# Performance work log

Hardware: AMD Instinct MI355X
Metric: run time of the kernel (lower is better)

Reference implementation:

```python
import jax, jax.numpy as jnp
import numpy as np

H1, C1 = 16, 8   # layer1 heads, per-head channels
H2, C2 = 16, 8   # layer2 heads, per-head channels
NEG_SLOPE = 0.2


def _gatv2_layer(x, src, dst, Wl, Wr, att, bias, n_nodes, H, C):
    # x: [N, F]; Wl/Wr: [F, H*C]; att: [H, C]; bias: [H*C]
    xl = (x @ Wl).reshape(n_nodes, H, C)  # source transform
    xr = (x @ Wr).reshape(n_nodes, H, C)  # target transform
    e = jax.nn.leaky_relu(xl[src] + xr[dst], NEG_SLOPE)   # [E, H, C]
    logit = jnp.einsum('ehc,hc->eh', e, att)              # [E, H]
    # segment softmax over incoming edges of each target node
    m = jax.ops.segment_max(logit, dst, num_segments=n_nodes)  # [N, H]
    ex = jnp.exp(logit - m[dst])
    denom = jax.ops.segment_sum(ex, dst, num_segments=n_nodes)  # [N, H]
    alpha = ex / (denom[dst] + 1e-16)                     # [E, H]
    msg = xl[src] * alpha[..., None]                      # [E, H, C]
    out = jax.ops.segment_sum(msg, dst, num_segments=n_nodes)  # [N, H, C]
    return out.reshape(n_nodes, H * C) + bias


def setup_inputs() -> dict:
    key = jax.random.key(0)
    ks = jax.random.split(key, 10)
    N, E, F_IN = 50000, 800000, 128
    x = jax.random.normal(ks[0], (N, F_IN), dtype=jnp.float32)
    edge_index = jax.random.randint(ks[1], (2, E), 0, N, dtype=jnp.int32)
    s = 0.1
    return {
        'x': x,
        'edge_index': edge_index,
        'Wl1': jax.random.normal(ks[2], (F_IN, H1 * C1), dtype=jnp.float32) * s,
        'Wr1': jax.random.normal(ks[3], (F_IN, H1 * C1), dtype=jnp.float32) * s,
        'att1': jax.random.normal(ks[4], (H1, C1), dtype=jnp.float32) * s,
        'b1': jax.random.normal(ks[5], (H1 * C1,), dtype=jnp.float32) * s,
        'Wl2': jax.random.normal(ks[6], (H1 * C1, H2 * C2), dtype=jnp.float32) * s,
        'Wr2': jax.random.normal(ks[7], (H1 * C1, H2 * C2), dtype=jnp.float32) * s,
        'att2': jax.random.normal(ks[8], (H2, C2), dtype=jnp.float32) * s,
        'b2': jax.random.normal(ks[9], (H2 * C2,), dtype=jnp.float32) * s,
    }


def reference(x, edge_index, Wl1, Wr1, att1, b1, Wl2, Wr2, att2, b2):
    N = x.shape[0]
    # PyG GATv2Conv adds self-loops by default
    loops = jnp.arange(N, dtype=edge_index.dtype)
    src = jnp.concatenate([edge_index[0], loops])
    dst = jnp.concatenate([edge_index[1], loops])
    # eval mode: F.dropout(training=False) is identity
    h = _gatv2_layer(x, src, dst, Wl1, Wr1, att1, b1, N, H1, C1)
    h = jax.nn.elu(h)
    h = _gatv2_layer(h, src, dst, Wl2, Wr2, att2, b2, N, H2, C2)
    return jax.nn.log_softmax(h, axis=1)
```

## Files before the change

### kernel.cpp

```cpp
#include <hip/hip_runtime.h>

#define NEG_SLOPE 0.2f
#define BSHIFT 9
#define BNODES 512
#define EPB 2048
#define SCAP 10240
#define LOG2E 1.44269504088896340736f

typedef __attribute__((ext_vector_type(8))) short short8;
typedef __attribute__((ext_vector_type(4))) float f32x4;

__device__ inline ushort f2bf(float f) {
  uint u = __builtin_bit_cast(uint, f);
  uint r = (u + 0x7FFFu + ((u >> 16) & 1u)) >> 16;
  return (ushort)r;
}
__device__ inline float bclo(uint u) { return __builtin_bit_cast(float, u << 16); }
__device__ inline float bchi(uint u) { return __builtin_bit_cast(float, u & 0xFFFF0000u); }

__device__ inline float fast_exp2(float x) {
  float r;
  asm("v_exp_f32 %0, %1" : "=v"(r) : "v"(x));
  return r;
}

__global__ __launch_bounds__(256) void k_prep_pc(
    const float* __restrict__ Wl1, const float* __restrict__ Wr1,
    const float* __restrict__ Wl2, const float* __restrict__ Wr2,
    ushort* __restrict__ WT1, ushort* __restrict__ WT2,
    const int* __restrict__ edst, int E, int* __restrict__ gcount) {
  int bid = blockIdx.x;
  int t = threadIdx.x;
  if (bid < 256) {
    const float* Wa = (bid < 128) ? Wl1 : Wl2;
    const float* Wb = (bid < 128) ? Wr1 : Wr2;
    ushort* WT = (bid < 128) ? WT1 : WT2;
    int i = (bid & 127) * 256 + t;
    int n = i >> 7, k = i & 127;
    float v = (n < 128) ? Wa[k * 128 + n] : Wb[k * 128 + (n - 128)];
    WT[i] = f2bf(v);
  } else {
    __shared__ int hist[128];
    if (t < 128) hist[t] = 0;
    __syncthreads();
    int e0 = (bid - 256) * EPB;
#pragma unroll
    for (int k = 0; k < EPB / 256; ++k) {
      int e = e0 + k * 256 + t;
      if (e < E) atomicAdd(&hist[edst[e] >> BSHIFT], 1);
    }
    __syncthreads();
    if (t < 128 && hist[t] > 0) atomicAdd(&gcount[t], hist[t]);
  }
}

__global__ __launch_bounds__(256) void k_pscan(const int* __restrict__ gcount,
                                               int* __restrict__ bbase,
                                               int* __restrict__ gcursor, int nb) {
  __shared__ int tsum[256];
  int t = threadIdx.x;
  int v = (t < nb) ? gcount[t] : 0;
  tsum[t] = v;
  __syncthreads();
  for (int d = 1; d < 256; d <<= 1) {
    int x = (t >= d) ? tsum[t - d] : 0;
    __syncthreads();
    tsum[t] += x;
    __syncthreads();
  }
  int excl = tsum[t] - v;
  if (t < nb) { bbase[t] = excl; gcursor[t] = excl; }
  if (t == nb - 1) bbase[nb] = excl + v;
}

__global__ __launch_bounds__(256) void k_pscatter(const int* __restrict__ esrc,
                                                  const int* __restrict__ edst, int E,
                                                  int* __restrict__ gcursor,
                                                  uint* __restrict__ pairs) {
  __shared__ int hist[128], lbase[128], gbase[128];
  __shared__ int tsum[256];
  __shared__ uint stag[EPB];
  int t = threadIdx.x;
  if (t < 128) hist[t] = 0;
  __syncthreads();
  int e0 = blockIdx.x * EPB;
  int b[8], r[8];
  uint pp[8];
#pragma unroll
  for (int k = 0; k < 8; ++k) {
    int e = e0 + k * 256 + t;
    if (e < E) {
      int d = edst[e], s = esrc[e];
      pp[k] = ((uint)d << 16) | (uint)s;
      b[k] = d >> BSHIFT;
      r[k] = atomicAdd(&hist[b[k]], 1);
    } else b[k] = -1;
  }
  __syncthreads();
  int hv = (t < 128) ? hist[t] : 0;
  tsum[t] = hv;
  __syncthreads();
  for (int dd = 1; dd < 256; dd <<= 1) {
    int x = (t >= dd) ? tsum[t - dd] : 0;
    __syncthreads();
    tsum[t] += x;
    __syncthreads();
  }
  if (t < 128) lbase[t] = tsum[t] - hv;
  __syncthreads();
  int tot = tsum[255];
#pragma unroll
  for (int k = 0; k < 8; ++k)
    if (b[k] >= 0) stag[lbase[b[k]] + r[k]] = pp[k];
  if (t < 128 && hv > 0) gbase[t] = atomicAdd(&gcursor[t], hv);
  __syncthreads();
  for (int i = t; i < tot; i += 256) {
    uint p = stag[i];
    int bb = (int)(p >> (16 + BSHIFT));
    pairs[gbase[bb] + (i - lbase[bb])] = p;
  }
}

__global__ __launch_bounds__(256) void k_bsort(const uint* __restrict__ pairs,
                                               const int* __restrict__ bbase,
                                               int* __restrict__ csr, int* __restrict__ offs,
                                               int N, int nb) {
  __shared__ int hist[BNODES], cur[BNODES], tsum[256];
  __shared__ int sorted[SCAP];
  int t = threadIdx.x;
  int first = blockIdx.x << BSHIFT;
  int nn = min(BNODES, N - first);
  int base = bbase[blockIdx.x];
  int cnt = bbase[blockIdx.x + 1] - base;
  int cbase = blockIdx.x * SCAP;
  hist[t] = 0; hist[t + 256] = 0;
  __syncthreads();
  for (int i = t; i < cnt; i += 256)
    atomicAdd(&hist[(int)(pairs[base + i] >> 16) - first], 1);
  __syncthreads();
  int a0 = hist[2 * t], a1 = hist[2 * t + 1];
  int a0p = (a0 + 3) & ~3, a1p = (a1 + 3) & ~3;
  tsum[t] = a0p + a1p;
  __syncthreads();
  for (int dd = 1; dd < 256; dd <<= 1) {
    int x = (t >= dd) ? tsum[t - dd] : 0;
    __syncthreads();
    tsum[t] += x;
    __syncthreads();
  }
  int ex = tsum[t] - (a0p + a1p);
  cur[2 * t] = ex; cur[2 * t + 1] = ex + a0p;
  if (2 * t < nn)     offs[first + 2 * t]     = ((cbase + ex) << 8) | a0;
  if (2 * t + 1 < nn) offs[first + 2 * t + 1] = ((cbase + ex + a0p) << 8) | a1;
  __syncthreads();
  for (int i = t; i < cnt; i += 256) {
    uint p = pairs[base + i];
    int pos = atomicAdd(&cur[(int)(p >> 16) - first], 1);
    sorted[pos] = (int)(p & 0xFFFFu);
  }
  __syncthreads();
  int tot = tsum[255];
  for (int i = t; i < tot; i += 256) csr[cbase + i] = sorted[i];
}

template <bool F32IN>
__global__ __launch_bounds__(256) void k_gemm_mfma(
    const void* __restrict__ Xin, const ushort* __restrict__ WT,
    ushort* __restrict__ XLB, ushort* __restrict__ XRB, int N) {
  __shared__ ushort As[64 * 128];
  int tid = threadIdx.x;
  int lane = tid & 63;
  int w = tid >> 6;
  int n0 = blockIdx.x * 64;
  int wcol = w * 64;

  short8 bfrag[4][4];
#pragma unroll
  for (int nt = 0; nt < 4; ++nt)
#pragma unroll
    for (int ks = 0; ks < 4; ++ks)
      bfrag[nt][ks] = *reinterpret_cast<const short8*>(
          WT + (size_t)(wcol + nt * 16 + (lane & 15)) * 128 + ks * 32 + (lane >> 4) * 8);

#pragma unroll
  for (int it = 0; it < 4; ++it) {
    int flat = it * 256 + tid;
    int r = flat >> 4;
    int cb = (flat & 15) << 4;
    short8 v = {0, 0, 0, 0, 0, 0, 0, 0};
    int row = n0 + r;
    if (row < N) {
      if constexpr (F32IN) {
        const float* Xf = (const float*)Xin + (size_t)row * 128 + (cb >> 1);
        float4 f0 = *reinterpret_cast<const float4*>(Xf);
        float4 f1 = *reinterpret_cast<const float4*>(Xf + 4);
        v[0] = (short)f2bf(f0.x); v[1] = (short)f2bf(f0.y);
        v[2] = (short)f2bf(f0.z); v[3] = (short)f2bf(f0.w);
        v[4] = (short)f2bf(f1.x); v[5] = (short)f2bf(f1.y);
        v[6] = (short)f2bf(f1.z); v[7] = (short)f2bf(f1.w);
      } else {
        v = *reinterpret_cast<const short8*>((const ushort*)Xin +
                                             (size_t)row * 128 + (cb >> 1));
      }
    }
    *reinterpret_cast<short8*>(reinterpret_cast<char*>(As) + r * 256 +
                               (cb ^ ((r & 7) << 4))) = v;
  }
  __syncthreads();

  f32x4 acc[4][4];
#pragma unroll
  for (int mt = 0; mt < 4; ++mt)
#pragma unroll
    for (int nt = 0; nt < 4; ++nt) acc[mt][nt] = f32x4{0.f, 0.f, 0.f, 0.f};

#pragma unroll
  for (int ks = 0; ks < 4; ++ks) {
    short8 af[4];
#pragma unroll
    for (int mt = 0; mt < 4; ++mt) {
      int row = mt * 16 + (lane & 15);
      int cb = ks * 64 + (lane >> 4) * 16;
      af[mt] = *reinterpret_cast<const short8*>(
          reinterpret_cast<char*>(As) + row * 256 + (cb ^ ((row & 7) << 4)));
    }
#pragma unroll
    for (int mt = 0; mt < 4; ++mt)
#pragma unroll
      for (int nt = 0; nt < 4; ++nt)
        acc[mt][nt] = __builtin_amdgcn_mfma_f32_16x16x32_bf16(
            af[mt], bfrag[nt][ks], acc[mt][nt], 0, 0, 0);
  }

  ushort* dstp = (w < 2) ? XLB : XRB;
#pragma unroll
  for (int mt = 0; mt < 4; ++mt) {
    int rbase = n0 + mt * 16 + (lane >> 4) * 4;
#pragma unroll
    for (int nt = 0; nt < 4; ++nt) {
      int c = (wcol + nt * 16 + (lane & 15)) & 127;
#pragma unroll
      for (int r = 0; r < 4; ++r) {
        float v = acc[mt][nt][r];
        ushort mb = f2bf(v);
        uint ob = (uint)__shfl_xor((int)(uint)mb, 1);
        int row = rbase + r;
        if ((lane & 1) == 0 && row < N) {
          ushort2 st; st.x = mb; st.y = (ushort)ob;
          *reinterpret_cast<ushort2*>(dstp + (size_t)row * 128 + c) = st;
        }
      }
    }
  }
}

template <int MODE>
__global__ __launch_bounds__(256, 4) void k_aggregate(
    const ushort* __restrict__ XLB, const ushort* __restrict__ XRB,
    const int* __restrict__ offs, const int* __restrict__ csr,
    const float* __restrict__ att, const float* __restrict__ bias,
    void* __restrict__ OUTV, int N) {
  int tid = threadIdx.x;
  int lane = tid & 63;
  int grp = lane >> 4, li = lane & 15;
  int wid = (blockIdx.x * 256 + tid) >> 6;
  int node = (wid << 2) + grp;
  bool valid = node < N;
  int cnode = valid ? node : (N - 1);
  int ch = li << 3;

  float4 alo = *reinterpret_cast<const float4*>(att + ch);
  float4 ahi = *reinterpret_cast<const float4*>(att + ch + 4);
  const float C6 = 0.6f * LOG2E;
  float a60 = alo.x * C6, a61 = alo.y * C6, a62 = alo.z * C6, a63 = alo.w * C6;
  float a64 = ahi.x * C6, a65 = ahi.y * C6, a66 = ahi.z * C6, a67 = ahi.w * C6;
  const float TT = 0.66666667f;

  uint4 xru = *reinterpret_cast<const uint4*>(XRB + ((size_t)cnode << 7) + ch);
  float xr0 = bclo(xru.x), xr1 = bchi(xru.x), xr2 = bclo(xru.y), xr3 = bchi(xru.y);
  float xr4 = bclo(xru.z), xr5 = bchi(xru.z), xr6 = bclo(xru.w), xr7 = bchi(xru.w);

  float acc0 = 0.f, acc1 = 0.f, acc2 = 0.f, acc3 = 0.f;
  float acc4 = 0.f, acc5 = 0.f, acc6 = 0.f, acc7 = 0.f, den = 0.f;

  uint sd = (uint)offs[cnode];
  int e0 = (int)(sd >> 8);
  int deg = valid ? (int)(sd & 255u) : 0;
  int wmax = deg;
  wmax = max(wmax, __shfl_xor(wmax, 16));
  wmax = max(wmax, __shfl_xor(wmax, 32));
  int ITER = (wmax + 3) >> 2;

  const int4* csr4 = reinterpret_cast<const int4*>(csr + e0);

#define PROC(U4, ACT)                                                        \
  {                                                                          \
    float x0 = bclo((U4).x), x1 = bchi((U4).x);                              \
    float x2 = bclo((U4).y), x3 = bchi((U4).y);                              \
    float x4 = bclo((U4).z), x5 = bchi((U4).z);                              \
    float x6 = bclo((U4).w), x7 = bchi((U4).w);                              \
    float t0 = x0 + xr0, t1 = x1 + xr1, t2 = x2 + xr2, t3 = x3 + xr3;        \
    float t4 = x4 + xr4, t5 = x5 + xr5, t6 = x6 + xr6, t7 = x7 + xr7;        \
    float u0 = fmaf(fabsf(t0), TT, t0), u1 = fmaf(fabsf(t1), TT, t1);        \
    float u2 = fmaf(fabsf(t2), TT, t2), u3 = fmaf(fabsf(t3), TT, t3);        \
    float u4 = fmaf(fabsf(t4), TT, t4), u5 = fmaf(fabsf(t5), TT, t5);        \
    float u6 = fmaf(fabsf(t6), TT, t6), u7 = fmaf(fabsf(t7), TT, t7);        \
    float q = u0 * a60;                                                      \
    q = fmaf(u1, a61, q); q = fmaf(u2, a62, q); q = fmaf(u3, a63, q);        \
    q = fmaf(u4, a64, q); q = fmaf(u5, a65, q); q = fmaf(u6, a66, q);        \
    q = fmaf(u7, a67, q);                                                    \
    q = (ACT) ? q : -200.f;                                                  \
    float exv = fast_exp2(q);                                                \
    acc0 = fmaf(exv, x0, acc0); acc1 = fmaf(exv, x1, acc1);                  \
    acc2 = fmaf(exv, x2, acc2); acc3 = fmaf(exv, x3, acc3);                  \
    acc4 = fmaf(exv, x4, acc4); acc5 = fmaf(exv, x5, acc5);                  \
    acc6 = fmaf(exv, x6, acc6); acc7 = fmaf(exv, x7, acc7);                  \
    den += exv;                                                              \
  }

#define GATHER(B0, B1, B2, B3, IDX, I0)                                      \
  {                                                                          \
    int s0_ = ((I0) < deg) ? (IDX).x : cnode;                                \
    int s1_ = ((I0) + 1 < deg) ? (IDX).y : cnode;                            \
    int s2_ = ((I0) + 2 < deg) ? (IDX).z : cnode;                            \
    int s3_ = ((I0) + 3 < deg) ? (IDX).w : cnode;                            \
    B0 = *reinterpret_cast<const uint4*>(XLB + (((size_t)(uint)s0_) << 7) + ch); \
    B1 = *reinterpret_cast<const uint4*>(XLB + (((size_t)(uint)s1_) << 7) + ch); \
    B2 = *reinterpret_cast<const uint4*>(XLB + (((size_t)(uint)s2_) << 7) + ch); \
    B3 = *reinterpret_cast<const uint4*>(XLB + (((size_t)(uint)s3_) << 7) + ch); \
  }

#define PROC4(B0, B1, B2, B3, I0)                                            \
  {                                                                          \
    PROC(B0, (I0) < deg); PROC(B1, (I0) + 1 < deg);                          \
    PROC(B2, (I0) + 2 < deg); PROC(B3, (I0) + 3 < deg);                      \
  }

  {
    uint4 us = *reinterpret_cast<const uint4*>(XLB + ((size_t)cnode << 7) + ch);
    PROC(us, valid);
  }

  uint4 A0, A1, A2, A3, B0, B1, B2, B3;
  int4 ia, ib;
  if (ITER > 0) {
    ia = csr4[0];
    GATHER(A0, A1, A2, A3, ia, 0);
    ib = (ITER > 1) ? csr4[1] : ia;
    int b = 1;
    for (; b + 1 < ITER; b += 2) {
      GATHER(B0, B1, B2, B3, ib, 4 * b);
      ia = csr4[b + 1];
      PROC4(A0, A1, A2, A3, 4 * (b - 1));
      GATHER(A0, A1, A2, A3, ia, 4 * (b + 1));
      ib = csr4[b + 2];
      PROC4(B0, B1, B2, B3, 4 * b);
    }
    if (b < ITER) {
      GATHER(B0, B1, B2, B3, ib, 4 * b);
      PROC4(A0, A1, A2, A3, 4 * (b - 1));
      PROC4(B0, B1, B2, B3, 4 * b);
    } else {
      PROC4(A0, A1, A2, A3, 4 * (b - 1));
    }
  }
#undef GATHER
#undef PROC4
#undef PROC

  float inv = 1.f / (den + 1e-16f);
  float4 blo = *reinterpret_cast<const float4*>(bias + ch);
  float4 bhi = *reinterpret_cast<const float4*>(bias + ch + 4);
  float v0 = acc0 * inv + blo.x, v1 = acc1 * inv + blo.y;
  float v2 = acc2 * inv + blo.z, v3 = acc3 * inv + blo.w;
  float v4 = acc4 * inv + bhi.x, v5 = acc5 * inv + bhi.y;
  float v6 = acc6 * inv + bhi.z, v7 = acc7 * inv + bhi.w;

  if (MODE == 0) {
    v0 = (v0 > 0.f) ? v0 : expm1f(v0); v1 = (v1 > 0.f) ? v1 : expm1f(v1);
    v2 = (v2 > 0.f) ? v2 : expm1f(v2); v3 = (v3 > 0.f) ? v3 : expm1f(v3);
    v4 = (v4 > 0.f) ? v4 : expm1f(v4); v5 = (v5 > 0.f) ? v5 : expm1f(v5);
    v6 = (v6 > 0.f) ? v6 : expm1f(v6); v7 = (v7 > 0.f) ? v7 : expm1f(v7);
    if (valid) {
      ushort u[8] = {f2bf(v0), f2bf(v1), f2bf(v2), f2bf(v3),
                     f2bf(v4), f2bf(v5), f2bf(v6), f2bf(v7)};
      *reinterpret_cast<uint4*>((ushort*)OUTV + ((size_t)node << 7) + ch) =
          *reinterpret_cast<uint4*>(u);
    }
  } else {
    float m = fmaxf(fmaxf(fmaxf(v0, v1), fmaxf(v2, v3)),
                    fmaxf(fmaxf(v4, v5), fmaxf(v6, v7)));
#pragma unroll
    for (int d = 1; d < 16; d <<= 1) m = fmaxf(m, __shfl_xor(m, d));
    float s = __expf(v0 - m) + __expf(v1 - m) + __expf(v2 - m) + __expf(v3 - m) +
              __expf(v4 - m) + __expf(v5 - m) + __expf(v6 - m) + __expf(v7 - m);
#pragma unroll
    for (int d = 1; d < 16; d <<= 1) s += __shfl_xor(s, d);
    float lse = m + logf(s);
    float* op = (float*)OUTV + ((size_t)node << 7) + ch;
    if (valid) {
      *reinterpret_cast<float4*>(op) =
          make_float4(v0 - lse, v1 - lse, v2 - lse, v3 - lse);
      *reinterpret_cast<float4*>(op + 4) =
          make_float4(v4 - lse, v5 - lse, v6 - lse, v7 - lse);
    }
  }
}

extern "C" void kernel_launch(void* const* d_in, const int* in_sizes, int n_in,
                              void* d_out, int out_size, void* d_ws, size_t ws_size,
                              hipStream_t stream) {
  const float* x    = (const float*)d_in[0];
  const int*   ei   = (const int*)d_in[1];
  const float* Wl1  = (const float*)d_in[2];
  const float* Wr1  = (const float*)d_in[3];
  const float* att1 = (const float*)d_in[4];
  const float* b1   = (const float*)d_in[5];
  const float* Wl2  = (const float*)d_in[6];
  const float* Wr2  = (const float*)d_in[7];
  const float* att2 = (const float*)d_in[8];
  const float* b2   = (const float*)d_in[9];

  int N = in_sizes[0] / 128;
  int E = in_sizes[1] / 2;
  const int* esrc = ei;
  const int* edst = ei + E;
  int nb = (N + BNODES - 1) >> BSHIFT;

  char* base = (char*)d_ws;
  size_t off = 0;
  auto take = [&](size_t bytes) {
    char* p = base + off;
    off = (off + bytes + 255) & ~(size_t)255;
    return p;
  };
  int*    offs    = (int*)take((size_t)N * 4);
  int*    csr     = (int*)take((size_t)nb * SCAP * 4 + 256);
  uint*   pairs   = (uint*)take((size_t)E * 4);
  int*    gcount  = (int*)take(128 * 4);
  int*    bbase   = (int*)take(132 * 4);
  int*    gcursor = (int*)take(128 * 4);
  ushort* XB      = (ushort*)take((size_t)N * 128 * 2);
  ushort* XLB     = (ushort*)take((size_t)N * 128 * 2);
  ushort* XRB     = (ushort*)take((size_t)N * 128 * 2);
  ushort* WT1     = (ushort*)take((size_t)256 * 128 * 2);
  ushort* WT2     = (ushort*)take((size_t)256 * 128 * 2);
  float*  OUT     = (float*)d_out;

  int pblocks = (E + EPB - 1) / EPB;
  int gblocks = (N + 63) / 64;
  int ablocks = (N + 15) / 16;

  hipMemsetAsync(gcount, 0, 128 * sizeof(int), stream);
  k_prep_pc<<<256 + pblocks, 256, 0, stream>>>(Wl1, Wr1, Wl2, Wr2, WT1, WT2,
                                               edst, E, gcount);
  k_pscan<<<1, 256, 0, stream>>>(gcount, bbase, gcursor, nb);
  k_pscatter<<<pblocks, 256, 0, stream>>>(esrc, edst, E, gcursor, pairs);
  k_bsort<<<nb, 256, 0, stream>>>(pairs, bbase, csr, offs, N, nb);

  k_gemm_mfma<true><<<gblocks, 256, 0, stream>>>(x, WT1, XLB, XRB, N);
  k_aggregate<0><<<ablocks, 256, 0, stream>>>(XLB, XRB, offs, csr, att1, b1, XB, N);
  k_gemm_mfma<false><<<gblocks, 256, 0, stream>>>(XB, WT2, XLB, XRB, N);
  k_aggregate<1><<<ablocks, 256, 0, stream>>>(XLB, XRB, offs, csr, att2, b2, OUT, N);
}
```

Baseline: 167.6 us.

## Fuse edge histogram with layer-1 GEMM and drop weight pre-transpose kernel

Removes the separate weight transpose/bf16 conversion pass: each GEMM block now reads the fp32 weights directly with a strided gather and converts them in registers. The destination-bucket histogram and the layer-1 GEMM run in one launch, with block ranges split between the two roles, which saves a launch and lets the two overlap. Bucket size is halved to 256 nodes (256 buckets), which changes the scatter, scan and bucket-sort shapes and shrinks the per-block shared staging. The trade-off is strided, uncoalesced weight loads repeated in every GEMM block, plus more buckets to handle.

```diff
diff --git a/kernel.cpp b/kernel.cpp
--- a/kernel.cpp
+++ b/kernel.cpp
@@ -1,10 +1,10 @@
 #include <hip/hip_runtime.h>
 
 #define NEG_SLOPE 0.2f
-#define BSHIFT 9
-#define BNODES 512
+#define BSHIFT 8
+#define BNODES 256
 #define EPB 2048
-#define SCAP 10240
+#define SCAP 5632
 #define LOG2E 1.44269504088896340736f
 
 typedef __attribute__((ext_vector_type(8))) short short8;
@@ -24,163 +24,33 @@
   return r;
 }
 
-__global__ __launch_bounds__(256) void k_prep_pc(
-    const float* __restrict__ Wl1, const float* __restrict__ Wr1,
-    const float* __restrict__ Wl2, const float* __restrict__ Wr2,
-    ushort* __restrict__ WT1, ushort* __restrict__ WT2,
-    const int* __restrict__ edst, int E, int* __restrict__ gcount) {
-  int bid = blockIdx.x;
-  int t = threadIdx.x;
-  if (bid < 256) {
-    const float* Wa = (bid < 128) ? Wl1 : Wl2;
-    const float* Wb = (bid < 128) ? Wr1 : Wr2;
-    ushort* WT = (bid < 128) ? WT1 : WT2;
-    int i = (bid & 127) * 256 + t;
-    int n = i >> 7, k = i & 127;
-    float v = (n < 128) ? Wa[k * 128 + n] : Wb[k * 128 + (n - 128)];
-    WT[i] = f2bf(v);
-  } else {
-    __shared__ int hist[128];
-    if (t < 128) hist[t] = 0;
-    __syncthreads();
-    int e0 = (bid - 256) * EPB;
-#pragma unroll
-    for (int k = 0; k < EPB / 256; ++k) {
-      int e = e0 + k * 256 + t;
-      if (e < E) atomicAdd(&hist[edst[e] >> BSHIFT], 1);
-    }
-    __syncthreads();
-    if (t < 128 && hist[t] > 0) atomicAdd(&gcount[t], hist[t]);
-  }
-}
-
-__global__ __launch_bounds__(256) void k_pscan(const int* __restrict__ gcount,
-                                               int* __restrict__ bbase,
-                                               int* __restrict__ gcursor, int nb) {
-  __shared__ int tsum[256];
-  int t = threadIdx.x;
-  int v = (t < nb) ? gcount[t] : 0;
-  tsum[t] = v;
-  __syncthreads();
-  for (int d = 1; d < 256; d <<= 1) {
-    int x = (t >= d) ? tsum[t - d] : 0;
-    __syncthreads();
-    tsum[t] += x;
-    __syncthreads();
-  }
-  int excl = tsum[t] - v;
-  if (t < nb) { bbase[t] = excl; gcursor[t] = excl; }
-  if (t == nb - 1) bbase[nb] = excl + v;
-}
-
-__global__ __launch_bounds__(256) void k_pscatter(const int* __restrict__ esrc,
-                                                  const int* __restrict__ edst, int E,
-                                                  int* __restrict__ gcursor,
-                                                  uint* __restrict__ pairs) {
-  __shared__ int hist[128], lbase[128], gbase[128];
-  __shared__ int tsum[256];
-  __shared__ uint stag[EPB];
-  int t = threadIdx.x;
-  if (t < 128) hist[t] = 0;
-  __syncthreads();
-  int e0 = blockIdx.x * EPB;
-  int b[8], r[8];
-  uint pp[8];
-#pragma unroll
-  for (int k = 0; k < 8; ++k) {
-    int e = e0 + k * 256 + t;
-    if (e < E) {
-      int d = edst[e], s = esrc[e];
-      pp[k] = ((uint)d << 16) | (uint)s;
-      b[k] = d >> BSHIFT;
-      r[k] = atomicAdd(&hist[b[k]], 1);
-    } else b[k] = -1;
-  }
-  __syncthreads();
-  int hv = (t < 128) ? hist[t] : 0;
-  tsum[t] = hv;
-  __syncthreads();
-  for (int dd = 1; dd < 256; dd <<= 1) {
-    int x = (t >= dd) ? tsum[t - dd] : 0;
-    __syncthreads();
-    tsum[t] += x;
-    __syncthreads();
-  }
-  if (t < 128) lbase[t] = tsum[t] - hv;
-  __syncthreads();
-  int tot = tsum[255];
-#pragma unroll
-  for (int k = 0; k < 8; ++k)
-    if (b[k] >= 0) stag[lbase[b[k]] + r[k]] = pp[k];
-  if (t < 128 && hv > 0) gbase[t] = atomicAdd(&gcursor[t], hv);
-  __syncthreads();
-  for (int i = t; i < tot; i += 256) {
-    uint p = stag[i];
-    int bb = (int)(p >> (16 + BSHIFT));
-    pairs[gbase[bb] + (i - lbase[bb])] = p;
-  }
-}
-
-__global__ __launch_bounds__(256) void k_bsort(const uint* __restrict__ pairs,
-                                               const int* __restrict__ bbase,
-                                               int* __restrict__ csr, int* __restrict__ offs,
-                                               int N, int nb) {
-  __shared__ int hist[BNODES], cur[BNODES], tsum[256];
-  __shared__ int sorted[SCAP];
-  int t = threadIdx.x;
-  int first = blockIdx.x << BSHIFT;
-  int nn = min(BNODES, N - first);
-  int base = bbase[blockIdx.x];
-  int cnt = bbase[blockIdx.x + 1] - base;
-  int cbase = blockIdx.x * SCAP;
-  hist[t] = 0; hist[t + 256] = 0;
-  __syncthreads();
-  for (int i = t; i < cnt; i += 256)
-    atomicAdd(&hist[(int)(pairs[base + i] >> 16) - first], 1);
-  __syncthreads();
-  int a0 = hist[2 * t], a1 = hist[2 * t + 1];
-  int a0p = (a0 + 3) & ~3, a1p = (a1 + 3) & ~3;
-  tsum[t] = a0p + a1p;
-  __syncthreads();
-  for (int dd = 1; dd < 256; dd <<= 1) {
-    int x = (t >= dd) ? tsum[t - dd] : 0;
-    __syncthreads();
-    tsum[t] += x;
-    __syncthreads();
-  }
-  int ex = tsum[t] - (a0p + a1p);
-  cur[2 * t] = ex; cur[2 * t + 1] = ex + a0p;
-  if (2 * t < nn)     offs[first + 2 * t]     = ((cbase + ex) << 8) | a0;
-  if (2 * t + 1 < nn) offs[first + 2 * t + 1] = ((cbase + ex + a0p) << 8) | a1;
-  __syncthreads();
-  for (int i = t; i < cnt; i += 256) {
-    uint p = pairs[base + i];
-    int pos = atomicAdd(&cur[(int)(p >> 16) - first], 1);
-    sorted[pos] = (int)(p & 0xFFFFu);
-  }
-  __syncthreads();
-  int tot = tsum[255];
-  for (int i = t; i < tot; i += 256) csr[cbase + i] = sorted[i];
-}
-
 template <bool F32IN>
-__global__ __launch_bounds__(256) void k_gemm_mfma(
-    const void* __restrict__ Xin, const ushort* __restrict__ WT,
-    ushort* __restrict__ XLB, ushort* __restrict__ XRB, int N) {
+__device__ __forceinline__ void gemm_body(
+    const void* __restrict__ Xin, const float* __restrict__ Wa,
+    const float* __restrict__ Wb, ushort* __restrict__ XLB,
+    ushort* __restrict__ XRB, int N, int gb) {
   __shared__ ushort As[64 * 128];
   int tid = threadIdx.x;
   int lane = tid & 63;
   int w = tid >> 6;
-  int n0 = blockIdx.x * 64;
+  int n0 = gb * 64;
   int wcol = w * 64;
 
   short8 bfrag[4][4];
 #pragma unroll
-  for (int nt = 0; nt < 4; ++nt)
-#pragma unroll
-    for (int ks = 0; ks < 4; ++ks)
-      bfrag[nt][ks] = *reinterpret_cast<const short8*>(
-          WT + (size_t)(wcol + nt * 16 + (lane & 15)) * 128 + ks * 32 + (lane >> 4) * 8);
+  for (int nt = 0; nt < 4; ++nt) {
+    int n = wcol + nt * 16 + (lane & 15);
+    const float* Wp = (n < 128) ? (Wa + n) : (Wb + (n - 128));
+#pragma unroll
+    for (int ks = 0; ks < 4; ++ks) {
+      int k0 = ks * 32 + (lane >> 4) * 8;
+      short8 v;
+#pragma unroll
+      for (int j = 0; j < 8; ++j)
+        v[j] = (short)f2bf(Wp[(size_t)(k0 + j) * 128]);
+      bfrag[nt][ks] = v;
+    }
+  }
 
 #pragma unroll
   for (int it = 0; it < 4; ++it) {
@@ -252,6 +122,145 @@
       }
     }
   }
+}
+
+__global__ __launch_bounds__(256) void k_fused1(
+    const int* __restrict__ edst, int E, int* __restrict__ gcount,
+    const float* __restrict__ X, const float* __restrict__ Wl1,
+    const float* __restrict__ Wr1, ushort* __restrict__ XLB,
+    ushort* __restrict__ XRB, int N, int pblocks) {
+  int bid = blockIdx.x;
+  if (bid < pblocks) {
+    __shared__ int hist[BNODES];
+    int t = threadIdx.x;
+    hist[t] = 0;
+    __syncthreads();
+    int e0 = bid * EPB;
+#pragma unroll
+    for (int k = 0; k < EPB / 256; ++k) {
+      int e = e0 + k * 256 + t;
+      if (e < E) atomicAdd(&hist[edst[e] >> BSHIFT], 1);
+    }
+    __syncthreads();
+    if (hist[t] > 0) atomicAdd(&gcount[t], hist[t]);
+  } else {
+    gemm_body<true>(X, Wl1, Wr1, XLB, XRB, N, bid - pblocks);
+  }
+}
+
+__global__ __launch_bounds__(256) void k_gemm2(
+    const ushort* __restrict__ XB, const float* __restrict__ Wl2,
+    const float* __restrict__ Wr2, ushort* __restrict__ XLB,
+    ushort* __restrict__ XRB, int N) {
+  gemm_body<false>(XB, Wl2, Wr2, XLB, XRB, N, blockIdx.x);
+}
+
+__global__ __launch_bounds__(256) void k_pscan(const int* __restrict__ gcount,
+                                               int* __restrict__ bbase,
+                                               int* __restrict__ gcursor, int nb) {
+  __shared__ int tsum[256];
+  int t = threadIdx.x;
+  int v = (t < nb) ? gcount[t] : 0;
+  tsum[t] = v;
+  __syncthreads();
+  for (int d = 1; d < 256; d <<= 1) {
+    int x = (t >= d) ? tsum[t - d] : 0;
+    __syncthreads();
+    tsum[t] += x;
+    __syncthreads();
+  }
+  int excl = tsum[t] - v;
+  if (t < nb) { bbase[t] = excl; gcursor[t] = excl; }
+  if (t == nb - 1) bbase[nb] = excl + v;
+}
+
+__global__ __launch_bounds__(256) void k_pscatter(const int* __restrict__ esrc,
+                                                  const int* __restrict__ edst, int E,
+                                                  int* __restrict__ gcursor,
+                                                  uint* __restrict__ pairs) {
+  __shared__ int hist[BNODES], lbase[BNODES], gbase[BNODES];
+  __shared__ int tsum[256];
+  __shared__ uint stag[EPB];
+  int t = threadIdx.x;
+  hist[t] = 0;
+  __syncthreads();
+  int e0 = blockIdx.x * EPB;
+  int b[8], r[8];
+  uint pp[8];
+#pragma unroll
+  for (int k = 0; k < 8; ++k) {
+    int e = e0 + k * 256 + t;
+    if (e < E) {
+      int d = edst[e], s = esrc[e];
+      pp[k] = ((uint)d << 16) | (uint)s;
+      b[k] = d >> BSHIFT;
+      r[k] = atomicAdd(&hist[b[k]], 1);
+    } else b[k] = -1;
+  }
+  __syncthreads();
+  int hv = hist[t];
+  tsum[t] = hv;
+  __syncthreads();
+  for (int dd = 1; dd < 256; dd <<= 1) {
+    int x = (t >= dd) ? tsum[t - dd] : 0;
+    __syncthreads();
+    tsum[t] += x;
+    __syncthreads();
+  }
+  lbase[t] = tsum[t] - hv;
+  __syncthreads();
+  int tot = tsum[255];
+#pragma unroll
+  for (int k = 0; k < 8; ++k)
+    if (b[k] >= 0) stag[lbase[b[k]] + r[k]] = pp[k];
+  if (hv > 0) gbase[t] = atomicAdd(&gcursor[t], hv);
+  __syncthreads();
+  for (int i = t; i < tot; i += 256) {
+    uint p = stag[i];
+    int bb = (int)(p >> 24);
+    pairs[gbase[bb] + (i - lbase[bb])] = p;
+  }
+}
+
+__global__ __launch_bounds__(256) void k_bsort(const uint* __restrict__ pairs,
+                                               const int* __restrict__ bbase,
+                                               int* __restrict__ csr, int* __restrict__ offs,
+                                               int N, int nb) {
+  __shared__ int hist[BNODES], cur[BNODES], tsum[256];
+  __shared__ int sorted[SCAP];
+  int t = threadIdx.x;
+  int first = blockIdx.x << BSHIFT;
+  int nn = min(BNODES, N - first);
+  int base = bbase[blockIdx.x];
+  int cnt = bbase[blockIdx.x + 1] - base;
+  int cbase = blockIdx.x * SCAP;
+  hist[t] = 0;
+  __syncthreads();
+  for (int i = t; i < cnt; i += 256)
+    atomicAdd(&hist[(int)(pairs[base + i] >> 16) - first], 1);
+  __syncthreads();
+  int a = hist[t];
+  int ap = (a + 3) & ~3;
+  tsum[t] = ap;
+  __syncthreads();
+  for (int dd = 1; dd < 256; dd <<= 1) {
+    int x = (t >= dd) ? tsum[t - dd] : 0;
+    __syncthreads();
+    tsum[t] += x;
+    __syncthreads();
+  }
+  int ex = tsum[t] - ap;
+  cur[t] = ex;
+  if (t < nn) offs[first + t] = ((cbase + ex) << 8) | a;
+  __syncthreads();
+  for (int i = t; i < cnt; i += 256) {
+    uint p = pairs[base + i];
+    int pos = atomicAdd(&cur[(int)(p >> 16) - first], 1);
+    sorted[pos] = (int)(p & 0xFFFFu);
+  }
+  __syncthreads();
+  int tot = tsum[255];
+  for (int i = t; i < tot; i += 256) csr[cbase + i] = sorted[i];
 }
 
 template <int MODE>
@@ -437,29 +446,26 @@
   int*    offs    = (int*)take((size_t)N * 4);
   int*    csr     = (int*)take((size_t)nb * SCAP * 4 + 256);
   uint*   pairs   = (uint*)take((size_t)E * 4);
-  int*    gcount  = (int*)take(128 * 4);
-  int*    bbase   = (int*)take(132 * 4);
-  int*    gcursor = (int*)take(128 * 4);
+  int*    gcount  = (int*)take(256 * 4);
+  int*    bbase   = (int*)take(260 * 4);
+  int*    gcursor = (int*)take(256 * 4);
   ushort* XB      = (ushort*)take((size_t)N * 128 * 2);
   ushort* XLB     = (ushort*)take((size_t)N * 128 * 2);
   ushort* XRB     = (ushort*)take((size_t)N * 128 * 2);
-  ushort* WT1     = (ushort*)take((size_t)256 * 128 * 2);
-  ushort* WT2     = (ushort*)take((size_t)256 * 128 * 2);
   float*  OUT     = (float*)d_out;
 
   int pblocks = (E + EPB - 1) / EPB;
   int gblocks = (N + 63) / 64;
   int ablocks = (N + 15) / 16;
 
-  hipMemsetAsync(gcount, 0, 128 * sizeof(int), stream);
-  k_prep_pc<<<256 + pblocks, 256, 0, stream>>>(Wl1, Wr1, Wl2, Wr2, WT1, WT2,
-                                               edst, E, gcount);
+  hipMemsetAsync(gcount, 0, 256 * sizeof(int), stream);
+  k_fused1<<<pblocks + gblocks, 256, 0, stream>>>(edst, E, gcount, x, Wl1, Wr1,
+                                                  XLB, XRB, N, pblocks);
   k_pscan<<<1, 256, 0, stream>>>(gcount, bbase, gcursor, nb);
   k_pscatter<<<pblocks, 256, 0, stream>>>(esrc, edst, E, gcursor, pairs);
   k_bsort<<<nb, 256, 0, stream>>>(pairs, bbase, csr, offs, N, nb);
 
-  k_gemm_mfma<true><<<gblocks, 256, 0, stream>>>(x, WT1, XLB, XRB, N);
   k_aggregate<0><<<ablocks, 256, 0, stream>>>(XLB, XRB, offs, csr, att1, b1, XB, N);
-  k_gemm_mfma<false><<<gblocks, 256, 0, stream>>>(XB, WT2, XLB, XRB, N);
+  k_gemm2<<<gblocks, 256, 0, stream>>>(XB, Wl2, Wr2, XLB, XRB, N);
   k_aggregate<1><<<ablocks, 256, 0, stream>>>(XLB, XRB, offs, csr, att2, b2, OUT, N);
 }
```

After: 178.6 us. 1.07x slower.
